# Optimization experiments

Hardware: AMD Instinct MI355X
Metric: run time of the kernel (lower is better)

## Reference

```python
import jax, jax.numpy as jnp
import numpy as np

N, DEG, F = 500000, 16, 128
H1, H2, OUT = 256, 256, 128


def setup_inputs() -> dict:
    key = jax.random.key(0)
    ks = jax.random.split(key, 8)
    s = lambda fan_in: 1.0 / np.sqrt(fan_in)
    return {
        "message": jax.random.normal(ks[0], (N, DEG, F), dtype=jnp.float32),
        "features": jax.random.normal(ks[1], (N, F), dtype=jnp.float32),
        "global_features": jax.random.normal(ks[2], (N, F), dtype=jnp.float32),
        "W1": jax.random.normal(ks[3], (3 * F, H1), dtype=jnp.float32) * s(3 * F),
        "b1": jnp.zeros((H1,), dtype=jnp.float32),
        "W2": jax.random.normal(ks[4], (H1, H2), dtype=jnp.float32) * s(H1),
        "b2": jnp.zeros((H2,), dtype=jnp.float32),
        "W3": jax.random.normal(ks[5], (H2, OUT), dtype=jnp.float32) * s(H2),
        "b3": jnp.zeros((OUT,), dtype=jnp.float32),
    }


def reference(message, features, global_features, W1, b1, W2, b2, W3, b3):
    # mailbox sum-aggregate over neighbors: [N, deg, F] -> [N, F]
    agg = jnp.sum(message, axis=1)
    # concat aggregated messages with node + global features: [N, 3F]
    x = jnp.concatenate([agg, features, global_features], axis=1)
    # MLP: Linear+ReLU, Linear+ReLU, Linear
    h = jax.nn.relu(x @ W1 + b1)
    h = jax.nn.relu(h @ W2 + b2)
    out = h @ W3 + b3
    # row-wise L2 (Frobenius over dim=1) normalization
    norm = jnp.linalg.norm(out, axis=1, keepdims=True)
    return out / (norm + 1e-8)
```

## Files before the change

kernel.cpp:

```cpp
#include <hip/hip_runtime.h>


typedef short short8   __attribute__((ext_vector_type(8)));
typedef short short4_t __attribute__((ext_vector_type(4)));
typedef float f32x4    __attribute__((ext_vector_type(4)));

#define SWZ(row, off) ((off) ^ (((row) & 7) << 4))

__device__ __forceinline__ unsigned short f2bf(float f) {
    unsigned int u = __float_as_uint(f);
    u += 0x7fffu + ((u >> 16) & 1u);
    return (unsigned short)(u >> 16);
}

__global__ void prep_weights(const float* __restrict__ W1,
                             const float* __restrict__ W2,
                             const float* __restrict__ W3,
                             short* __restrict__ pw1,
                             short* __restrict__ pw2,
                             short* __restrict__ pw3) {
    int idx = blockIdx.x * 256 + threadIdx.x;
    if (idx < 98304) {
        int j = idx & 7, l = (idx >> 3) & 63, g = idx >> 9;
        int ks = g % 12, tn = g / 12;
        int n = tn * 16 + (l & 15);
        int k = ks * 32 + ((l >> 4) << 3) + j;
        pw1[idx] = (short)f2bf(W1[k * 256 + n]);
    } else if (idx < 98304 + 65536) {
        int e = idx - 98304;
        int j = e & 7, l = (e >> 3) & 63, g = e >> 9;
        int ks = g & 7, tn = g >> 3;
        int n = tn * 16 + (l & 15);
        int k = ks * 32 + ((l >> 4) << 3) + j;
        pw2[e] = (short)f2bf(W2[k * 256 + n]);
    } else if (idx < 98304 + 65536 + 32768) {
        int e = idx - 98304 - 65536;
        int j = e & 7, l = (e >> 3) & 63, g = e >> 9;
        int ks = g & 7, tn = g >> 3;
        int n = tn * 16 + (l & 15);
        int k = ks * 32 + ((l >> 4) << 3) + j;
        pw3[e] = (short)f2bf(W3[k * 128 + n]);
    }
}

__global__ __launch_bounds__(256) void agg_kernel(
    const float* __restrict__ msg, short* __restrict__ agg, int n_rows)
{
    const int w = threadIdx.x >> 6;
    const int l = threadIdx.x & 63;
    const long long pb = (long long)blockIdx.x * 8 + 2 * w;
    if (pb >= n_rows) return;

    const f32x4* base = (const f32x4*)((const char*)msg + pb * 8192);
    f32x4 tA[8], tB[8];
    const bool okB = (pb + 1) < n_rows;
    #pragma unroll
    for (int i = 0; i < 8; ++i) tA[i] = __builtin_nontemporal_load(base + i * 64 + l);
    if (okB) {
        #pragma unroll
        for (int i = 0; i < 8; ++i) tB[i] = __builtin_nontemporal_load(base + (8 + i) * 64 + l);
    } else {
        #pragma unroll
        for (int i = 0; i < 8; ++i) tB[i] = (f32x4){0.f, 0.f, 0.f, 0.f};
    }
    f32x4 sA = ((tA[0] + tA[1]) + (tA[2] + tA[3])) + ((tA[4] + tA[5]) + (tA[6] + tA[7]));
    f32x4 sB = ((tB[0] + tB[1]) + (tB[2] + tB[3])) + ((tB[4] + tB[5]) + (tB[6] + tB[7]));
    #pragma unroll
    for (int c = 0; c < 4; ++c) {
        sA[c] += __shfl_xor(sA[c], 32);
        sB[c] += __shfl_xor(sB[c], 32);
    }
    f32x4 s = (l < 32) ? sA : sB;
    short4_t s4;
    s4[0] = (short)f2bf(s[0]); s4[1] = (short)f2bf(s[1]);
    s4[2] = (short)f2bf(s[2]); s4[3] = (short)f2bf(s[3]);
    const long long orow = pb + (l >> 5);
    if (orow < n_rows)
        *(short4_t*)(agg + orow * 128 + (l & 31) * 4) = s4;
}

__global__ __launch_bounds__(256, 4) void node_net(
    const short* __restrict__ aggb,
    const float* __restrict__ feat,
    const float* __restrict__ glob,
    const float* __restrict__ b1v,
    const float* __restrict__ b2v,
    const float* __restrict__ b3v,
    const short* __restrict__ pw1,
    const short* __restrict__ pw2,
    const short* __restrict__ pw3,
    float* __restrict__ out,
    int n_rows)
{
    __shared__ char lds[40960];
    char* ldsH = lds + 24576;

    const int tid  = threadIdx.x;
    const int lane = tid & 63;
    const int w    = tid >> 6;
    const int lr   = lane & 15;
    const int lk   = lane >> 4;
    const long long r0 = (long long)blockIdx.x * 32;

    const f32x4 zero4 = {0.f, 0.f, 0.f, 0.f};

    short8 ring[3][4];
    #pragma unroll
    for (int k0 = 0; k0 < 3; ++k0)
        #pragma unroll
        for (int ci = 0; ci < 4; ++ci)
            ring[k0][ci] = *(const short8*)(pw1 + ((((w * 4 + ci) * 12 + k0) * 64 + lane) << 3));

    float bias1[4], bias2[4], bias3[2];
    #pragma unroll
    for (int ci = 0; ci < 4; ++ci) {
        bias1[ci] = b1v[w * 64 + ci * 16 + lr];
        bias2[ci] = b2v[w * 64 + ci * 16 + lr];
    }
    #pragma unroll
    for (int ci = 0; ci < 2; ++ci) bias3[ci] = b3v[w * 32 + ci * 16 + lr];

    f32x4 fr[4], gr[4];
    #pragma unroll
    for (int q = 0; q < 4; ++q) {
        int r = (tid >> 5) + q * 8;
        long long row = r0 + r;
        fr[q] = zero4; gr[q] = zero4;
        if (row < n_rows) {
            fr[q] = ((const f32x4*)feat)[row * 32 + (tid & 31)];
            gr[q] = ((const f32x4*)glob)[row * 32 + (tid & 31)];
        }
    }
    short8 av[2];
    #pragma unroll
    for (int pass = 0; pass < 2; ++pass) {
        int r = tid >> 3;
        long long row = r0 + r;
        av[pass] = (short8){0, 0, 0, 0, 0, 0, 0, 0};
        if (row < n_rows)
            av[pass] = *(const short8*)(aggb + row * 128 + ((tid & 7) + 8 * pass) * 8);
    }

    #pragma unroll
    for (int pass = 0; pass < 2; ++pass) {
        int r = tid >> 3;
        int c = (tid & 7) + 8 * pass;
        *(short8*)(lds + SWZ(r, r * 256 + c * 16)) = av[pass];
    }
    #pragma unroll
    for (int q = 0; q < 4; ++q) {
        int r = (tid >> 5) + q * 8;
        short4_t sf, sg;
        sf[0] = (short)f2bf(fr[q][0]); sf[1] = (short)f2bf(fr[q][1]);
        sf[2] = (short)f2bf(fr[q][2]); sf[3] = (short)f2bf(fr[q][3]);
        sg[0] = (short)f2bf(gr[q][0]); sg[1] = (short)f2bf(gr[q][1]);
        sg[2] = (short)f2bf(gr[q][2]); sg[3] = (short)f2bf(gr[q][3]);
        *(short4_t*)(lds + 8192  + SWZ(r, r * 256 + (tid & 31) * 8)) = sf;
        *(short4_t*)(lds + 16384 + SWZ(r, r * 256 + (tid & 31) * 8)) = sg;
    }
    __syncthreads();

    f32x4 acc1[2][4];
    #pragma unroll
    for (int ri = 0; ri < 2; ++ri)
        #pragma unroll
        for (int ci = 0; ci < 4; ++ci) acc1[ri][ci] = zero4;

    #pragma unroll
    for (int ks = 0; ks < 12; ++ks) {
        const int s = ks & 3, p = ks >> 2;
        short8 a[2];
        #pragma unroll
        for (int ri = 0; ri < 2; ++ri) {
            int row = ri * 16 + lr;
            a[ri] = *(const short8*)(lds + p * 8192 + SWZ(row, row * 256 + s * 64 + lk * 16));
        }
        #pragma unroll
        for (int ri = 0; ri < 2; ++ri)
            #pragma unroll
            for (int ci = 0; ci < 4; ++ci)
                acc1[ri][ci] = __builtin_amdgcn_mfma_f32_16x16x32_bf16(
                    a[ri], ring[ks % 3][ci], acc1[ri][ci], 0, 0, 0);
        if (ks < 9) {
            #pragma unroll
            for (int ci = 0; ci < 4; ++ci)
                ring[ks % 3][ci] = *(const short8*)(pw1 + ((((w * 4 + ci) * 12 + (ks + 3)) * 64 + lane) << 3));
        } else {
            #pragma unroll
            for (int ci = 0; ci < 4; ++ci)
                ring[ks % 3][ci] = *(const short8*)(pw2 + ((((w * 4 + ci) * 8 + (ks - 9)) * 64 + lane) << 3));
        }
    }

    #pragma unroll
    for (int ci = 0; ci < 4; ++ci) {
        int col = w * 64 + ci * 16 + lr;
        #pragma unroll
        for (int ri = 0; ri < 2; ++ri)
            #pragma unroll
            for (int i = 0; i < 4; ++i) {
                int row = ri * 16 + lk * 4 + i;
                float v = fmaxf(acc1[ri][ci][i] + bias1[ci], 0.f);
                *(short*)(ldsH + SWZ(row, row * 512 + col * 2)) = (short)f2bf(v);
            }
    }
    __syncthreads();

    f32x4 acc2[2][4];
    #pragma unroll
    for (int ri = 0; ri < 2; ++ri)
        #pragma unroll
        for (int ci = 0; ci < 4; ++ci) acc2[ri][ci] = zero4;

    #pragma unroll
    for (int ks = 0; ks < 8; ++ks) {
        short8 a[2];
        #pragma unroll
        for (int ri = 0; ri < 2; ++ri) {
            int row = ri * 16 + lr;
            a[ri] = *(const short8*)(ldsH + SWZ(row, row * 512 + ks * 64 + lk * 16));
        }
        #pragma unroll
        for (int ri = 0; ri < 2; ++ri)
            #pragma unroll
            for (int ci = 0; ci < 4; ++ci)
                acc2[ri][ci] = __builtin_amdgcn_mfma_f32_16x16x32_bf16(
                    a[ri], ring[ks % 3][ci], acc2[ri][ci], 0, 0, 0);
        if (ks < 5) {
            #pragma unroll
            for (int ci = 0; ci < 4; ++ci)
                ring[ks % 3][ci] = *(const short8*)(pw2 + ((((w * 4 + ci) * 8 + (ks + 3)) * 64 + lane) << 3));
        } else {
            #pragma unroll
            for (int ci = 0; ci < 2; ++ci)
                ring[ks % 3][ci] = *(const short8*)(pw3 + ((((w * 2 + ci) * 8 + (ks - 5)) * 64 + lane) << 3));
        }
    }

    #pragma unroll
    for (int ci = 0; ci < 4; ++ci) {
        int col = w * 64 + ci * 16 + lr;
        #pragma unroll
        for (int ri = 0; ri < 2; ++ri)
            #pragma unroll
            for (int i = 0; i < 4; ++i) {
                int row = ri * 16 + lk * 4 + i;
                float v = fmaxf(acc2[ri][ci][i] + bias2[ci], 0.f);
                *(short*)(lds + SWZ(row, row * 512 + col * 2)) = (short)f2bf(v);
            }
    }
    __syncthreads();

    f32x4 acc3[2][2];
    #pragma unroll
    for (int ri = 0; ri < 2; ++ri)
        #pragma unroll
        for (int ci = 0; ci < 2; ++ci) acc3[ri][ci] = zero4;

    #pragma unroll
    for (int ks = 0; ks < 8; ++ks) {
        short8 a[2];
        #pragma unroll
        for (int ri = 0; ri < 2; ++ri) {
            int row = ri * 16 + lr;
            a[ri] = *(const short8*)(lds + SWZ(row, row * 512 + ks * 64 + lk * 16));
        }
        #pragma unroll
        for (int ri = 0; ri < 2; ++ri)
            #pragma unroll
            for (int ci = 0; ci < 2; ++ci)
                acc3[ri][ci] = __builtin_amdgcn_mfma_f32_16x16x32_bf16(
                    a[ri], ring[(ks + 2) % 3][ci], acc3[ri][ci], 0, 0, 0);
        if (ks < 5) {
            #pragma unroll
            for (int ci = 0; ci < 2; ++ci)
                ring[(ks + 2) % 3][ci] = *(const short8*)(pw3 + ((((w * 2 + ci) * 8 + (ks + 3)) * 64 + lane) << 3));
        }
    }

    #pragma unroll
    for (int ci = 0; ci < 2; ++ci) {
        int col = w * 32 + ci * 16 + lr;
        #pragma unroll
        for (int ri = 0; ri < 2; ++ri)
            #pragma unroll
            for (int i = 0; i < 4; ++i) {
                int row = ri * 16 + lk * 4 + i;
                float v = acc3[ri][ci][i] + bias3[ci];
                *(float*)(ldsH + SWZ(row, row * 512 + col * 4)) = v;
            }
    }
    __syncthreads();

    #pragma unroll
    for (int pass = 0; pass < 4; ++pass) {
        const int r  = (tid >> 5) + pass * 8;
        const int fl = tid & 31;
        f32x4 v = *(const f32x4*)(ldsH + SWZ(r, r * 512 + fl * 16));
        float ss = v[0]*v[0] + v[1]*v[1] + v[2]*v[2] + v[3]*v[3];
        ss += __shfl_xor(ss, 1, 32);
        ss += __shfl_xor(ss, 2, 32);
        ss += __shfl_xor(ss, 4, 32);
        ss += __shfl_xor(ss, 8, 32);
        ss += __shfl_xor(ss, 16, 32);
        float inv = 1.f / (sqrtf(ss) + 1e-8f);
        long long row = r0 + r;
        if (row < n_rows) {
            f32x4 o = v * inv;
            ((f32x4*)out)[row * 32 + fl] = o;
        }
    }
}

extern "C" void kernel_launch(void* const* d_in, const int* in_sizes, int n_in,
                              void* d_out, int out_size, void* d_ws, size_t ws_size,
                              hipStream_t stream) {
    const float* msg  = (const float*)d_in[0];
    const float* feat = (const float*)d_in[1];
    const float* glob = (const float*)d_in[2];
    const float* W1   = (const float*)d_in[3];
    const float* b1   = (const float*)d_in[4];
    const float* W2   = (const float*)d_in[5];
    const float* b2   = (const float*)d_in[6];
    const float* W3   = (const float*)d_in[7];
    const float* b3   = (const float*)d_in[8];
    float* out = (float*)d_out;

    const int n_rows = in_sizes[1] / 128;

    short* pw1  = (short*)d_ws;
    short* pw2  = pw1 + 98304;
    short* pw3  = pw2 + 65536;
    short* aggb = pw3 + 32768;

    hipLaunchKernelGGL(prep_weights, dim3(768), dim3(256), 0, stream,
                       W1, W2, W3, pw1, pw2, pw3);

    const int ablocks = (n_rows + 7) / 8;
    hipLaunchKernelGGL(agg_kernel, dim3(ablocks), dim3(256), 0, stream,
                       msg, aggb, n_rows);

    const int nblocks = (n_rows + 31) / 32;
    hipLaunchKernelGGL(node_net, dim3(nblocks), dim3(256), 0, stream,
                       aggb, feat, glob, b1, b2, b3, pw1, pw2, pw3, out, n_rows);
}
```

Measured before the change: 1.328 ms.

## Double node_net row tile to 64 and drop weight register ring prefetch

The MLP kernel now processes 64 rows per block instead of 32, so each weight fragment loaded from global memory feeds twice as many MFMAs. The three-slot register ring that prefetched weights ahead is removed; weights are now loaded per k-step right before use. LDS grows to 48KB with one buffer reused across layers, which adds barriers, and launch bounds drop to 3 blocks per CU. The change cuts weight reload traffic but loses the explicit prefetch latency hiding and reduces occupancy.

```diff
diff --git a/kernel.cpp b/kernel.cpp
--- a/kernel.cpp
+++ b/kernel.cpp
@@ -79,7 +79,7 @@
         *(short4_t*)(agg + orow * 128 + (l & 31) * 4) = s4;
 }
 
-__global__ __launch_bounds__(256, 4) void node_net(
+__global__ __launch_bounds__(256, 3) void node_net(
     const short* __restrict__ aggb,
     const float* __restrict__ feat,
     const float* __restrict__ glob,
@@ -92,24 +92,16 @@
     float* __restrict__ out,
     int n_rows)
 {
-    __shared__ char lds[40960];
-    char* ldsH = lds + 24576;
+    __shared__ char lds[49152];
 
     const int tid  = threadIdx.x;
     const int lane = tid & 63;
     const int w    = tid >> 6;
     const int lr   = lane & 15;
     const int lk   = lane >> 4;
-    const long long r0 = (long long)blockIdx.x * 32;
+    const long long r0 = (long long)blockIdx.x * 64;
 
     const f32x4 zero4 = {0.f, 0.f, 0.f, 0.f};
-
-    short8 ring[3][4];
-    #pragma unroll
-    for (int k0 = 0; k0 < 3; ++k0)
-        #pragma unroll
-        for (int ci = 0; ci < 4; ++ci)
-            ring[k0][ci] = *(const short8*)(pw1 + ((((w * 4 + ci) * 12 + k0) * 64 + lane) << 3));
 
     float bias1[4], bias2[4], bias3[2];
     #pragma unroll
@@ -120,128 +112,106 @@
     #pragma unroll
     for (int ci = 0; ci < 2; ++ci) bias3[ci] = b3v[w * 32 + ci * 16 + lr];
 
-    f32x4 fr[4], gr[4];
-    #pragma unroll
-    for (int q = 0; q < 4; ++q) {
-        int r = (tid >> 5) + q * 8;
+    #pragma unroll
+    for (int pass = 0; pass < 4; ++pass) {
+        int r = tid >> 2;
+        int c = (tid & 3) + 4 * pass;
         long long row = r0 + r;
-        fr[q] = zero4; gr[q] = zero4;
+        short8 v = {0, 0, 0, 0, 0, 0, 0, 0};
+        if (row < n_rows) v = *(const short8*)(aggb + row * 128 + c * 8);
+        *(short8*)(lds + SWZ(r, r * 256 + c * 16)) = v;
+    }
+    #pragma unroll
+    for (int pass = 0; pass < 8; ++pass) {
+        int r = (tid >> 5) + pass * 8;
+        long long row = r0 + r;
+        f32x4 f = zero4, g = zero4;
         if (row < n_rows) {
-            fr[q] = ((const f32x4*)feat)[row * 32 + (tid & 31)];
-            gr[q] = ((const f32x4*)glob)[row * 32 + (tid & 31)];
-        }
-    }
-    short8 av[2];
-    #pragma unroll
-    for (int pass = 0; pass < 2; ++pass) {
-        int r = tid >> 3;
-        long long row = r0 + r;
-        av[pass] = (short8){0, 0, 0, 0, 0, 0, 0, 0};
-        if (row < n_rows)
-            av[pass] = *(const short8*)(aggb + row * 128 + ((tid & 7) + 8 * pass) * 8);
-    }
-
-    #pragma unroll
-    for (int pass = 0; pass < 2; ++pass) {
-        int r = tid >> 3;
-        int c = (tid & 7) + 8 * pass;
-        *(short8*)(lds + SWZ(r, r * 256 + c * 16)) = av[pass];
-    }
-    #pragma unroll
-    for (int q = 0; q < 4; ++q) {
-        int r = (tid >> 5) + q * 8;
+            f = ((const f32x4*)feat)[row * 32 + (tid & 31)];
+            g = ((const f32x4*)glob)[row * 32 + (tid & 31)];
+        }
         short4_t sf, sg;
-        sf[0] = (short)f2bf(fr[q][0]); sf[1] = (short)f2bf(fr[q][1]);
-        sf[2] = (short)f2bf(fr[q][2]); sf[3] = (short)f2bf(fr[q][3]);
-        sg[0] = (short)f2bf(gr[q][0]); sg[1] = (short)f2bf(gr[q][1]);
-        sg[2] = (short)f2bf(gr[q][2]); sg[3] = (short)f2bf(gr[q][3]);
-        *(short4_t*)(lds + 8192  + SWZ(r, r * 256 + (tid & 31) * 8)) = sf;
-        *(short4_t*)(lds + 16384 + SWZ(r, r * 256 + (tid & 31) * 8)) = sg;
-    }
-    __syncthreads();
-
-    f32x4 acc1[2][4];
-    #pragma unroll
-    for (int ri = 0; ri < 2; ++ri)
+        sf[0] = (short)f2bf(f[0]); sf[1] = (short)f2bf(f[1]);
+        sf[2] = (short)f2bf(f[2]); sf[3] = (short)f2bf(f[3]);
+        sg[0] = (short)f2bf(g[0]); sg[1] = (short)f2bf(g[1]);
+        sg[2] = (short)f2bf(g[2]); sg[3] = (short)f2bf(g[3]);
+        *(short4_t*)(lds + 16384 + SWZ(r, r * 256 + (tid & 31) * 8)) = sf;
+        *(short4_t*)(lds + 32768 + SWZ(r, r * 256 + (tid & 31) * 8)) = sg;
+    }
+    __syncthreads();
+
+    f32x4 acc1[4][4];
+    #pragma unroll
+    for (int ri = 0; ri < 4; ++ri)
         #pragma unroll
         for (int ci = 0; ci < 4; ++ci) acc1[ri][ci] = zero4;
 
     #pragma unroll
     for (int ks = 0; ks < 12; ++ks) {
-        const int s = ks & 3, p = ks >> 2;
-        short8 a[2];
-        #pragma unroll
-        for (int ri = 0; ri < 2; ++ri) {
+        const int p = ks >> 2, s = ks & 3;
+        short8 a[4], b[4];
+        #pragma unroll
+        for (int ri = 0; ri < 4; ++ri) {
             int row = ri * 16 + lr;
-            a[ri] = *(const short8*)(lds + p * 8192 + SWZ(row, row * 256 + s * 64 + lk * 16));
-        }
-        #pragma unroll
-        for (int ri = 0; ri < 2; ++ri)
+            a[ri] = *(const short8*)(lds + p * 16384 + SWZ(row, row * 256 + s * 64 + lk * 16));
+        }
+        #pragma unroll
+        for (int ci = 0; ci < 4; ++ci)
+            b[ci] = *(const short8*)(pw1 + ((((w * 4 + ci) * 12 + ks) * 64 + lane) << 3));
+        #pragma unroll
+        for (int ri = 0; ri < 4; ++ri)
             #pragma unroll
             for (int ci = 0; ci < 4; ++ci)
                 acc1[ri][ci] = __builtin_amdgcn_mfma_f32_16x16x32_bf16(
-                    a[ri], ring[ks % 3][ci], acc1[ri][ci], 0, 0, 0);
-        if (ks < 9) {
-            #pragma unroll
-            for (int ci = 0; ci < 4; ++ci)
-                ring[ks % 3][ci] = *(const short8*)(pw1 + ((((w * 4 + ci) * 12 + (ks + 3)) * 64 + lane) << 3));
-        } else {
-            #pragma unroll
-            for (int ci = 0; ci < 4; ++ci)
-                ring[ks % 3][ci] = *(const short8*)(pw2 + ((((w * 4 + ci) * 8 + (ks - 9)) * 64 + lane) << 3));
-        }
-    }
+                    a[ri], b[ci], acc1[ri][ci], 0, 0, 0);
+    }
+    __syncthreads();
 
     #pragma unroll
     for (int ci = 0; ci < 4; ++ci) {
         int col = w * 64 + ci * 16 + lr;
         #pragma unroll
-        for (int ri = 0; ri < 2; ++ri)
+        for (int ri = 0; ri < 4; ++ri)
             #pragma unroll
             for (int i = 0; i < 4; ++i) {
                 int row = ri * 16 + lk * 4 + i;
                 float v = fmaxf(acc1[ri][ci][i] + bias1[ci], 0.f);
-                *(short*)(ldsH + SWZ(row, row * 512 + col * 2)) = (short)f2bf(v);
+                *(short*)(lds + SWZ(row, row * 512 + col * 2)) = (short)f2bf(v);
             }
     }
     __syncthreads();
 
-    f32x4 acc2[2][4];
-    #pragma unroll
-    for (int ri = 0; ri < 2; ++ri)
+    f32x4 acc2[4][4];
+    #pragma unroll
+    for (int ri = 0; ri < 4; ++ri)
         #pragma unroll
         for (int ci = 0; ci < 4; ++ci) acc2[ri][ci] = zero4;
 
     #pragma unroll
     for (int ks = 0; ks < 8; ++ks) {
-        short8 a[2];
-        #pragma unroll
-        for (int ri = 0; ri < 2; ++ri) {
+        short8 a[4], b[4];
+        #pragma unroll
+        for (int ri = 0; ri < 4; ++ri) {
             int row = ri * 16 + lr;
-            a[ri] = *(const short8*)(ldsH + SWZ(row, row * 512 + ks * 64 + lk * 16));
-        }
-        #pragma unroll
-        for (int ri = 0; ri < 2; ++ri)
+            a[ri] = *(const short8*)(lds + SWZ(row, row * 512 + ks * 64 + lk * 16));
+        }
+        #pragma unroll
+        for (int ci = 0; ci < 4; ++ci)
+            b[ci] = *(const short8*)(pw2 + ((((w * 4 + ci) * 8 + ks) * 64 + lane) << 3));
+        #pragma unroll
+        for (int ri = 0; ri < 4; ++ri)
             #pragma unroll
             for (int ci = 0; ci < 4; ++ci)
                 acc2[ri][ci] = __builtin_amdgcn_mfma_f32_16x16x32_bf16(
-                    a[ri], ring[ks % 3][ci], acc2[ri][ci], 0, 0, 0);
-        if (ks < 5) {
-            #pragma unroll
-            for (int ci = 0; ci < 4; ++ci)
-                ring[ks % 3][ci] = *(const short8*)(pw2 + ((((w * 4 + ci) * 8 + (ks + 3)) * 64 + lane) << 3));
-        } else {
-            #pragma unroll
-            for (int ci = 0; ci < 2; ++ci)
-                ring[ks % 3][ci] = *(const short8*)(pw3 + ((((w * 2 + ci) * 8 + (ks - 5)) * 64 + lane) << 3));
-        }
-    }
+                    a[ri], b[ci], acc2[ri][ci], 0, 0, 0);
+    }
+    __syncthreads();
 
     #pragma unroll
     for (int ci = 0; ci < 4; ++ci) {
         int col = w * 64 + ci * 16 + lr;
         #pragma unroll
-        for (int ri = 0; ri < 2; ++ri)
+        for (int ri = 0; ri < 4; ++ri)
             #pragma unroll
             for (int i = 0; i < 4; ++i) {
                 int row = ri * 16 + lk * 4 + i;
@@ -251,52 +221,51 @@
     }
     __syncthreads();
 
-    f32x4 acc3[2][2];
-    #pragma unroll
-    for (int ri = 0; ri < 2; ++ri)
+    f32x4 acc3[4][2];
+    #pragma unroll
+    for (int ri = 0; ri < 4; ++ri)
         #pragma unroll
         for (int ci = 0; ci < 2; ++ci) acc3[ri][ci] = zero4;
 
     #pragma unroll
     for (int ks = 0; ks < 8; ++ks) {
-        short8 a[2];
-        #pragma unroll
-        for (int ri = 0; ri < 2; ++ri) {
+        short8 a[4], b[2];
+        #pragma unroll
+        for (int ri = 0; ri < 4; ++ri) {
             int row = ri * 16 + lr;
             a[ri] = *(const short8*)(lds + SWZ(row, row * 512 + ks * 64 + lk * 16));
         }
         #pragma unroll
-        for (int ri = 0; ri < 2; ++ri)
+        for (int ci = 0; ci < 2; ++ci)
+            b[ci] = *(const short8*)(pw3 + ((((w * 2 + ci) * 8 + ks) * 64 + lane) << 3));
+        #pragma unroll
+        for (int ri = 0; ri < 4; ++ri)
             #pragma unroll
             for (int ci = 0; ci < 2; ++ci)
                 acc3[ri][ci] = __builtin_amdgcn_mfma_f32_16x16x32_bf16(
-                    a[ri], ring[(ks + 2) % 3][ci], acc3[ri][ci], 0, 0, 0);
-        if (ks < 5) {
-            #pragma unroll
-            for (int ci = 0; ci < 2; ++ci)
-                ring[(ks + 2) % 3][ci] = *(const short8*)(pw3 + ((((w * 2 + ci) * 8 + (ks + 3)) * 64 + lane) << 3));
-        }
-    }
+                    a[ri], b[ci], acc3[ri][ci], 0, 0, 0);
+    }
+    __syncthreads();
 
     #pragma unroll
     for (int ci = 0; ci < 2; ++ci) {
         int col = w * 32 + ci * 16 + lr;
         #pragma unroll
-        for (int ri = 0; ri < 2; ++ri)
+        for (int ri = 0; ri < 4; ++ri)
             #pragma unroll
             for (int i = 0; i < 4; ++i) {
                 int row = ri * 16 + lk * 4 + i;
                 float v = acc3[ri][ci][i] + bias3[ci];
-                *(float*)(ldsH + SWZ(row, row * 512 + col * 4)) = v;
+                *(float*)(lds + SWZ(row, row * 512 + col * 4)) = v;
             }
     }
     __syncthreads();
 
     #pragma unroll
-    for (int pass = 0; pass < 4; ++pass) {
+    for (int pass = 0; pass < 8; ++pass) {
         const int r  = (tid >> 5) + pass * 8;
         const int fl = tid & 31;
-        f32x4 v = *(const f32x4*)(ldsH + SWZ(r, r * 512 + fl * 16));
+        f32x4 v = *(const f32x4*)(lds + SWZ(r, r * 512 + fl * 16));
         float ss = v[0]*v[0] + v[1]*v[1] + v[2]*v[2] + v[3]*v[3];
         ss += __shfl_xor(ss, 1, 32);
         ss += __shfl_xor(ss, 2, 32);
@@ -340,7 +309,7 @@
     hipLaunchKernelGGL(agg_kernel, dim3(ablocks), dim3(256), 0, stream,
                        msg, aggb, n_rows);
 
-    const int nblocks = (n_rows + 31) / 32;
+    const int nblocks = (n_rows + 63) / 64;
     hipLaunchKernelGGL(node_net, dim3(nblocks), dim3(256), 0, stream,
                        aggb, feat, glob, b1, b2, b3, pw1, pw2, pw3, out, n_rows);
 }
```

Result: slower. 1.440 ms (+8.4%).
